# Optimization experiments

Measured on AMD Instinct MI355X. Metric: run time of the kernel, lower is better.

## Reference

```python
import jax, jax.numpy as jnp
import numpy as np

B, T, C = 2, 2048, 1024
H = 16
D = C // H  # head_dim = 64


def setup_inputs() -> dict:
    key = jax.random.key(0)
    k1, k2, k3, k4, k5 = jax.random.split(key, 5)
    s = 1.0 / np.sqrt(C)
    return {
        "x": jax.random.normal(k1, (B, T, C), dtype=jnp.float32),
        "w_qkv": jax.random.normal(k2, (C, 3 * C), dtype=jnp.float32) * s,
        "b_qkv": jax.random.normal(k3, (3 * C,), dtype=jnp.float32) * 0.01,
        "w_out": jax.random.normal(k4, (C, C), dtype=jnp.float32) * s,
        "b_out": jax.random.normal(k5, (C,), dtype=jnp.float32) * 0.01,
    }


def reference(x, w_qkv, b_qkv, w_out, b_out):
    Bx, Tx, Cx = x.shape
    qkv = x @ w_qkv + b_qkv                      # [B,T,3C]
    qkv = qkv.reshape(Bx, Tx, 3, H, D)
    q, k, v = qkv[:, :, 0], qkv[:, :, 1], qkv[:, :, 2]  # [B,T,H,D]
    # [B,H,T,T] scores with scaling
    scores = jnp.einsum("bqhd,bkhd->bhqk", q, k) / np.sqrt(D).astype(np.float32)
    causal = jnp.tril(jnp.ones((Tx, Tx), dtype=bool))
    scores = jnp.where(causal[None, None], scores, -jnp.inf)
    attn = jax.nn.softmax(scores, axis=-1)
    out = jnp.einsum("bhqk,bkhd->bqhd", attn, v).reshape(Bx, Tx, Cx)
    return out @ w_out + b_out
```

## Files before the change

### kernel.cpp

```cpp
#include <hip/hip_runtime.h>
#include <stdint.h>

typedef unsigned short u16;
typedef __attribute__((ext_vector_type(8))) short bfrag;
typedef __attribute__((ext_vector_type(4))) short bfrag4;
typedef __attribute__((ext_vector_type(4))) float f32x4;

#define MFMA_BF16 __builtin_amdgcn_mfma_f32_16x16x32_bf16

static constexpr int Bc = 2;
static constexpr int Tc = 2048;
static constexpr int Cc = 1024;
static constexpr int Hc = 16;
static constexpr int Dc = 64;
static constexpr int N3 = 3 * Cc;

__device__ __forceinline__ u16 f2bf(float f) {
    union { unsigned int i; float f; } v; v.f = f;
    unsigned int u = v.i;
    u += 0x7fffu + ((u >> 16) & 1u);
    return (u16)(u >> 16);
}
__device__ __forceinline__ unsigned int fbits(float f) {
    union { unsigned int i; float f; } v; v.f = f; return v.i;
}
__device__ __forceinline__ unsigned int pack_bf2(float hi, float lo) {
    return __builtin_amdgcn_perm(fbits(hi), fbits(lo), 0x07060302u);
}

#if __has_builtin(__builtin_amdgcn_mfma_f32_16x16x16bf16_1k)
__device__ __forceinline__ f32x4 MFMA16(bfrag4 a, bfrag4 b, f32x4 c) {
    return __builtin_amdgcn_mfma_f32_16x16x16bf16_1k(a, b, c, 0, 0, 0);
}
#elif __has_builtin(__builtin_amdgcn_mfma_f32_16x16x16_bf16)
__device__ __forceinline__ f32x4 MFMA16(bfrag4 a, bfrag4 b, f32x4 c) {
    return __builtin_amdgcn_mfma_f32_16x16x16_bf16(a, b, c, 0, 0, 0);
}
#else
__device__ __forceinline__ f32x4 MFMA16(bfrag4 a, bfrag4 b, f32x4 c) {
    bfrag a8 = {a[0], a[1], a[2], a[3], 0, 0, 0, 0};
    bfrag b8 = {b[0], b[1], b[2], b[3], 0, 0, 0, 0};
    return MFMA_BF16(a8, b8, c, 0, 0, 0);
}
#endif

__device__ __forceinline__ void async_load16(const u16* g, u16* lds) {
    __builtin_amdgcn_global_load_lds(
        (const __attribute__((address_space(1))) unsigned int*)g,
        (__attribute__((address_space(3))) unsigned int*)lds, 16, 0, 0);
}

__global__ __launch_bounds__(256) void prep(
    const float* __restrict__ x, const float* __restrict__ w_qkv,
    const float* __restrict__ w_out, u16* __restrict__ xb,
    u16* __restrict__ WqkvT, u16* __restrict__ WoutT) {
    __shared__ u16 tile[32][33];
    const int blk = blockIdx.x, tid = threadIdx.x;
    if (blk < 4096) {
        const int i = (blk * 256 + tid) * 4;
        const float4 v = *(const float4*)(x + i);
        ushort4 o;
        o.x = f2bf(v.x); o.y = f2bf(v.y); o.z = f2bf(v.z); o.w = f2bf(v.w);
        *(ushort4*)(xb + i) = o;
        return;
    }
    const int tx = tid & 31, ty = tid >> 5;
    const float* in; u16* out; int rows, cols, c0, r0;
    if (blk < 4096 + 3072) {
        const int t = blk - 4096;
        in = w_qkv; out = WqkvT; rows = 1024; cols = 3072;
        c0 = (t % 96) * 32; r0 = (t / 96) * 32;
    } else {
        const int t = blk - 7168;
        in = w_out; out = WoutT; rows = 1024; cols = 1024;
        c0 = (t & 31) * 32; r0 = (t >> 5) * 32;
    }
    for (int i = 0; i < 4; i++)
        tile[ty + 8 * i][tx] = f2bf(in[(size_t)(r0 + ty + 8 * i) * cols + c0 + tx]);
    __syncthreads();
    for (int i = 0; i < 4; i++)
        out[(size_t)(c0 + ty + 8 * i) * rows + r0 + tx] = tile[tx][ty + 8 * i];
}

__global__ void transpose_v(const u16* __restrict__ P, u16* __restrict__ Vt) {
    __shared__ u16 tile[32][33];
    const int bh = blockIdx.z, b = bh >> 4, h = bh & 15;
    const int t0 = blockIdx.x * 32, d0 = blockIdx.y * 32;
    const int tx = threadIdx.x, ty = threadIdx.y;
    const u16* src = P + (size_t)b * Tc * N3 + 2 * Cc + h * Dc;
    for (int i = 0; i < 4; i++)
        tile[ty + 8 * i][tx] = src[(size_t)(t0 + ty + 8 * i) * N3 + d0 + tx];
    __syncthreads();
    u16* dst = Vt + ((size_t)bh * Dc) * Tc;
    for (int i = 0; i < 4; i++)
        dst[(size_t)(d0 + ty + 8 * i) * Tc + t0 + tx] = tile[tx][ty + 8 * i];
}

template <int MODE>
__global__ __launch_bounds__(256) void gemm_bt(
    const u16* __restrict__ A, const u16* __restrict__ BT,
    const float* __restrict__ bias, void* __restrict__ out_p,
    int M, int Nn, int K) {
    __shared__ __align__(16) u16 As[2][128 * 32];
    __shared__ __align__(16) u16 Bs[2][128 * 32];

    const int tid  = threadIdx.x;
    const int wave = tid >> 6, lane = tid & 63;
    const int quad = lane >> 4, l16 = lane & 15;
    const int wm = wave & 1, wn = wave >> 1;
    const int m0 = blockIdx.y * 128, n0 = blockIdx.x * 128;

    f32x4 acc[4][4];
    #pragma unroll
    for (int i = 0; i < 4; i++)
        #pragma unroll
        for (int j = 0; j < 4; j++)
            acc[i][j] = (f32x4){0.f, 0.f, 0.f, 0.f};

    const int rloc = 2 * (lane >> 3) + ((lane >> 2) & 1);
    const int cg   = ((lane & 3) ^ ((lane >> 3) & 3)) * 8;
    const int rk   = (l16 >> 1) & 3;
    const int rodd = (l16 & 1) * 32;

    const int T = K >> 5;
    #define STAGE(t, bsel)                                                      \
        {                                                                       \
            const int k0_ = (t) << 5;                                           \
            _Pragma("unroll")                                                   \
            for (int j = 0; j < 2; j++) {                                       \
                const int R0 = wave * 32 + j * 16;                              \
                async_load16(A  + (size_t)(m0 + R0 + rloc) * K + k0_ + cg,      \
                             &As[bsel][R0 * 32]);                               \
                async_load16(BT + (size_t)(n0 + R0 + rloc) * K + k0_ + cg,      \
                             &Bs[bsel][R0 * 32]);                               \
            }                                                                   \
        }

    STAGE(0, 0);
    for (int t = 0; t < T; t++) {
        __syncthreads();
        if (t + 1 < T) STAGE(t + 1, (t + 1) & 1);
        const u16* Ab = As[t & 1];
        const u16* Bb = Bs[t & 1];
        bfrag af[4], bf[4];
        #pragma unroll
        for (int mt = 0; mt < 4; mt++) {
            const int r = wm * 64 + mt * 16 + l16;
            af[mt] = *(const bfrag*)(Ab + (r >> 1) * 64 + rodd + (quad ^ rk) * 8);
        }
        #pragma unroll
        for (int nt = 0; nt < 4; nt++) {
            const int r = wn * 64 + nt * 16 + l16;
            bf[nt] = *(const bfrag*)(Bb + (r >> 1) * 64 + rodd + (quad ^ rk) * 8);
        }
        #pragma unroll
        for (int mt = 0; mt < 4; mt++)
            #pragma unroll
            for (int nt = 0; nt < 4; nt++)
                acc[mt][nt] = MFMA_BF16(af[mt], bf[nt], acc[mt][nt], 0, 0, 0);
    }
    #undef STAGE

    #pragma unroll
    for (int nt = 0; nt < 4; nt++) {
        const int gn = n0 + wn * 64 + nt * 16 + l16;
        const float bv = bias[gn];
        #pragma unroll
        for (int mt = 0; mt < 4; mt++) {
            #pragma unroll
            for (int r = 0; r < 4; r++) {
                const int gm = m0 + wm * 64 + mt * 16 + quad * 4 + r;
                if (MODE == 1)
                    ((u16*)out_p)[(size_t)gm * Nn + gn] = f2bf(acc[mt][nt][r] + bv);
                else
                    ((float*)out_p)[(size_t)gm * Nn + gn] = acc[mt][nt][r] + bv;
            }
        }
    }
}

__global__ __launch_bounds__(256, 4) void attn_kernel(
    const u16* __restrict__ QKVp, const u16* __restrict__ Vt,
    u16* __restrict__ Ob) {
    __shared__ __align__(16) u16 KsF[2][64 * 64];
    __shared__ __align__(16) u16 VsF[2][64 * 64];

    const int tid  = threadIdx.x;
    const int wave = tid >> 6, lane = tid & 63;
    const int quad = lane >> 4, l16 = lane & 15;

    const int bh = blockIdx.x & 31;
    const int jq = 31 - (blockIdx.x >> 5);
    const int b = bh >> 4, h = bh & 15;
    const u16* Qp = QKVp + (size_t)b * Tc * N3 + h * Dc;
    const u16* Kp = Qp + Cc;
    const u16* Vp = Vt + (size_t)bh * Dc * Tc;

    const int qw = jq * 64 + wave * 16;

    const int row8 = lane >> 3;
    const int swz  = ((lane & 7) ^ row8) * 8;
    const int pk0 = ((quad)     ^ (l16 & 7)) * 8;
    const int pk1 = ((quad + 4) ^ (l16 & 7)) * 8;

    bfrag qf0, qf1;
    {
        const u16* qp = Qp + (size_t)(qw + l16) * N3 + quad * 8;
        qf0 = *(const bfrag*)qp;
        qf1 = *(const bfrag*)(qp + 32);
    }

    float l_i = 0.f;
    f32x4 oacc[4];
    #pragma unroll
    for (int g = 0; g < 4; g++) oacc[g] = (f32x4){0.f, 0.f, 0.f, 0.f};

    #define STAGEKV(t, bsel)                                                    \
        {                                                                       \
            const int k0_ = (t) * 64;                                           \
            _Pragma("unroll")                                                   \
            for (int j = 0; j < 2; j++) {                                       \
                const int rr = wave * 16 + j * 8;                               \
                const int gr = rr + row8;                                       \
                async_load16(Kp + (size_t)(k0_ + gr) * N3 + swz,                \
                             &KsF[bsel][rr * 64]);                              \
                async_load16(Vp + (size_t)gr * Tc + k0_ + swz,                  \
                             &VsF[bsel][rr * 64]);                              \
            }                                                                   \
        }

    STAGEKV(0, 0);
    for (int t = 0; t <= jq; t++) {
        __syncthreads();
        if (t < jq) STAGEKV(t + 1, (t + 1) & 1);
        const u16* Kb = KsF[t & 1];
        const u16* Vb = VsF[t & 1];
        const int k0 = t * 64;
        (void)k0;

        f32x4 s[4];
        #pragma unroll
        for (int g = 0; g < 4; g++) {
            const u16* kb = Kb + (g * 16 + l16) * 64;
            bfrag kf0 = *(const bfrag*)(kb + pk0);
            bfrag kf1 = *(const bfrag*)(kb + pk1);
            f32x4 z = (f32x4){0.f, 0.f, 0.f, 0.f};
            z = MFMA_BF16(kf0, qf0, z, 0, 0, 0);
            z = MFMA_BF16(kf1, qf1, z, 0, 0, 0);
            s[g] = z;
        }

        #pragma unroll
        for (int g = 0; g < 4; g++)
            #pragma unroll
            for (int r = 0; r < 4; r++)
                s[g][r] = __expf(s[g][r] * 0.125f);
        if (t == jq) {
            #pragma unroll
            for (int g = 0; g < 4; g++)
                #pragma unroll
                for (int r = 0; r < 4; r++)
                    if (g * 16 + quad * 4 + r > wave * 16 + l16) s[g][r] = 0.f;
        }
        #pragma unroll
        for (int g = 0; g < 4; g++)
            l_i += s[g][0] + s[g][1] + s[g][2] + s[g][3];

        #pragma unroll
        for (int g = 0; g < 4; g++) {
            union { unsigned int u[2]; bfrag4 v; } pf;
            pf.u[0] = pack_bf2(s[g][1], s[g][0]);
            pf.u[1] = pack_bf2(s[g][3], s[g][2]);
            const int vc = ((2 * g + (quad >> 1)) ^ (l16 & 7)) * 8 + (quad & 1) * 4;
            #pragma unroll
            for (int ng = 0; ng < 4; ng++) {
                const bfrag4 vf = *(const bfrag4*)(Vb + (ng * 16 + l16) * 64 + vc);
                oacc[ng] = MFMA16(vf, pf.v, oacc[ng]);
            }
        }
    }
    #undef STAGEKV

    float rs = l_i;
    rs += __shfl_xor(rs, 16);
    rs += __shfl_xor(rs, 32);
    const float inv = 1.f / rs;
    const int q = qw + l16;
    u16* orow = Ob + (size_t)(b * Tc + q) * Cc + h * Dc + quad * 4;
    #pragma unroll
    for (int ng = 0; ng < 4; ng++) {
        ushort4 o;
        o.x = f2bf(oacc[ng][0] * inv);
        o.y = f2bf(oacc[ng][1] * inv);
        o.z = f2bf(oacc[ng][2] * inv);
        o.w = f2bf(oacc[ng][3] * inv);
        *(ushort4*)(orow + ng * 16) = o;
    }
}

extern "C" void kernel_launch(void* const* d_in, const int* in_sizes, int n_in,
                              void* d_out, int out_size, void* d_ws, size_t ws_size,
                              hipStream_t stream) {
    const float* x     = (const float*)d_in[0];
    const float* w_qkv = (const float*)d_in[1];
    const float* b_qkv = (const float*)d_in[2];
    const float* w_out = (const float*)d_in[3];
    const float* b_out = (const float*)d_in[4];
    float* out = (float*)d_out;
    u16* ws  = (u16*)d_ws;

    u16* xb    = ws;
    u16* WqkvT = xb    + (size_t)4096 * 1024;
    u16* WoutT = WqkvT + (size_t)3072 * 1024;
    u16* QKVp  = WoutT + (size_t)1024 * 1024;
    u16* Vt    = QKVp  + (size_t)4096 * 3072;
    u16* Ao    = xb;

    prep<<<8192, 256, 0, stream>>>(x, w_qkv, w_out, xb, WqkvT, WoutT);
    gemm_bt<1><<<dim3(3072 / 128, 4096 / 128), 256, 0, stream>>>(
        xb, WqkvT, b_qkv, QKVp, 4096, 3072, 1024);
    transpose_v<<<dim3(Tc / 32, Dc / 32, Bc * Hc), dim3(32, 8), 0, stream>>>(
        QKVp, Vt);
    attn_kernel<<<1024, 256, 0, stream>>>(QKVp, Vt, Ao);
    gemm_bt<0><<<dim3(1024 / 128, 4096 / 128), 256, 0, stream>>>(
        Ao, WoutT, b_out, out, 4096, 1024, 1024);
}
```

Before: 179.7 us.

## Use dedicated 128x384 triple-buffered 512-thread GEMM for QKV projection

Replaces the generic 128x128 double-buffered GEMM for the QKV projection with a specialized kernel using 128x384 tiles, 8 waves, and a three-stage async LDS pipeline with explicit vmcnt waits and MFMA priority boosts. Larger N tiles raise arithmetic intensity per A load and cut the grid to 256 blocks. The cost is 96KB of dynamic shared memory and 96 accumulators per thread, which may limit occupancy. The grid is also smaller relative to the CU count.

```diff
diff --git a/kernel.cpp b/kernel.cpp
--- a/kernel.cpp
+++ b/kernel.cpp
@@ -96,6 +96,98 @@
         dst[(size_t)(d0 + ty + 8 * i) * Tc + t0 + tx] = tile[tx][ty + 8 * i];
 }
 
+__global__ __launch_bounds__(512, 2) void gemm_qkv(
+    const u16* __restrict__ A, const u16* __restrict__ BT,
+    const float* __restrict__ bias, u16* __restrict__ out,
+    int M, int Nn, int K) {
+    extern __shared__ __align__(16) u16 smem[];
+    u16* As = smem;
+    u16* Bs = smem + 3 * (128 * 32);
+
+    const int tid  = threadIdx.x;
+    const int wave = tid >> 6, lane = tid & 63;
+    const int quad = lane >> 4, l16 = lane & 15;
+    const int wm = wave >> 2, wn = wave & 3;
+    const int m0 = blockIdx.y * 128, n0 = blockIdx.x * 384;
+
+    f32x4 acc[4][6];
+    #pragma unroll
+    for (int i = 0; i < 4; i++)
+        #pragma unroll
+        for (int j = 0; j < 6; j++)
+            acc[i][j] = (f32x4){0.f, 0.f, 0.f, 0.f};
+
+    const int rA = lane >> 2;
+    const int cA = ((lane & 3) ^ (rA & 3)) * 8;
+
+    const u16* Ag  = A  + (size_t)(m0 + wave * 16 + rA) * K + cA;
+    const u16* Bg0 = BT + (size_t)(n0 + wave * 48 + rA) * K + cA;
+    u16* ldsA = As + (wave * 16) * 32;
+    u16* ldsB = Bs + (wave * 48) * 32;
+
+    const int swz8 = (quad ^ (l16 & 3)) * 8;
+    int offA[4], offB[6];
+    #pragma unroll
+    for (int mt = 0; mt < 4; mt++)
+        offA[mt] = (wm * 64 + mt * 16 + l16) * 32 + swz8;
+    #pragma unroll
+    for (int nt = 0; nt < 6; nt++)
+        offB[nt] = (wn * 96 + nt * 16 + l16) * 32 + swz8;
+
+    #define STAGE_Q(t, bsel)                                                   \
+        {                                                                      \
+            const int k0_ = (t) << 5;                                          \
+            async_load16(Ag + k0_, ldsA + (bsel) * (128 * 32));                \
+            _Pragma("unroll")                                                  \
+            for (int j = 0; j < 3; j++)                                        \
+                async_load16(Bg0 + (size_t)(j * 16) * K + k0_,                 \
+                             ldsB + (bsel) * (384 * 32) + j * (16 * 32));      \
+        }
+
+    STAGE_Q(0, 0);
+    STAGE_Q(1, 1);
+
+    const int T = K >> 5;
+    for (int t = 0; t < T; t++) {
+        if (t + 1 < T) asm volatile("s_waitcnt vmcnt(4)" ::: "memory");
+        else           asm volatile("s_waitcnt vmcnt(0)" ::: "memory");
+        __builtin_amdgcn_s_barrier();
+        asm volatile("" ::: "memory");
+        if (t + 2 < T) { STAGE_Q(t + 2, (t + 2) % 3); }
+
+        const u16* Ab = As + (t % 3) * (128 * 32);
+        const u16* Bb = Bs + (t % 3) * (384 * 32);
+        bfrag af[4], bf[6];
+        #pragma unroll
+        for (int mt = 0; mt < 4; mt++) af[mt] = *(const bfrag*)(Ab + offA[mt]);
+        #pragma unroll
+        for (int nt = 0; nt < 6; nt++) bf[nt] = *(const bfrag*)(Bb + offB[nt]);
+
+        __builtin_amdgcn_s_setprio(1);
+        #pragma unroll
+        for (int mt = 0; mt < 4; mt++)
+            #pragma unroll
+            for (int nt = 0; nt < 6; nt++)
+                acc[mt][nt] = MFMA_BF16(af[mt], bf[nt], acc[mt][nt], 0, 0, 0);
+        __builtin_amdgcn_s_setprio(0);
+    }
+    #undef STAGE_Q
+
+    #pragma unroll
+    for (int nt = 0; nt < 6; nt++) {
+        const int gn = n0 + wn * 96 + nt * 16 + l16;
+        const float bv = bias[gn];
+        #pragma unroll
+        for (int mt = 0; mt < 4; mt++) {
+            #pragma unroll
+            for (int r = 0; r < 4; r++) {
+                const int gm = m0 + wm * 64 + mt * 16 + quad * 4 + r;
+                out[(size_t)gm * Nn + gn] = f2bf(acc[mt][nt][r] + bv);
+            }
+        }
+    }
+}
+
 template <int MODE>
 __global__ __launch_bounds__(256) void gemm_bt(
     const u16* __restrict__ A, const u16* __restrict__ BT,
@@ -235,8 +327,6 @@
         if (t < jq) STAGEKV(t + 1, (t + 1) & 1);
         const u16* Kb = KsF[t & 1];
         const u16* Vb = VsF[t & 1];
-        const int k0 = t * 64;
-        (void)k0;
 
         f32x4 s[4];
         #pragma unroll
@@ -316,8 +406,16 @@
     u16* Vt    = QKVp  + (size_t)4096 * 3072;
     u16* Ao    = xb;
 
+    static bool smem_set = false;
+    if (!smem_set) {
+        hipFuncSetAttribute(reinterpret_cast<const void*>(gemm_qkv),
+                            hipFuncAttributeMaxDynamicSharedMemorySize,
+                            96 * 1024);
+        smem_set = true;
+    }
+
     prep<<<8192, 256, 0, stream>>>(x, w_qkv, w_out, xb, WqkvT, WoutT);
-    gemm_bt<1><<<dim3(3072 / 128, 4096 / 128), 256, 0, stream>>>(
+    gemm_qkv<<<dim3(3072 / 384, 4096 / 128), 512, 96 * 1024, stream>>>(
         xb, WqkvT, b_qkv, QKVp, 4096, 3072, 1024);
     transpose_v<<<dim3(Tc / 32, Dc / 32, Bc * Hc), dim3(32, 8), 0, stream>>>(
         QKVp, Vt);
```

Result: no change. 178.4 us (-0.7%).
